# Optimization experiments

Measured on AMD Instinct MI355X. Metric: run time of the kernel, lower is better.

The kernel has to match this reference:

```python
import jax, jax.numpy as jnp
import numpy as np

B, S, T = 64, 256, 32
VS, VT = 4000, 32000
E = H = 512
L = 2
PAD_IDX = 1
BOS_IDX = 2


def setup_inputs() -> dict:
    key = jax.random.key(0)
    ks = jax.random.split(key, 16)
    u = lambda k, sh: jax.random.uniform(k, sh, jnp.float32, -0.08, 0.08)
    inp = {
        'X': jax.random.randint(ks[0], (B, S), 0, VS),
        'y': jax.random.randint(ks[1], (B, T), 0, VT),
        'emb_src': u(ks[2], (VS, E)).at[PAD_IDX].set(0.0),
        'emb_tgt': u(ks[3], (VT, E)).at[PAD_IDX].set(0.0),
        'enc_Wih': u(ks[4], (L, 4 * H, E)),
        'enc_Whh': u(ks[5], (L, 4 * H, H)),
        'enc_bih': u(ks[6], (L, 4 * H)),
        'enc_bhh': u(ks[7], (L, 4 * H)),
        'dec_Wih': u(ks[8], (L, 4 * H, E)),
        'dec_Whh': u(ks[9], (L, 4 * H, H)),
        'dec_bih': u(ks[10], (L, 4 * H)),
        'dec_bhh': u(ks[11], (L, 4 * H)),
        'fcW': u(ks[12], (VT, H)),
        'fcb': u(ks[13], (VT,)),
    }
    return inp


def _cell(x, h, c, Wih, Whh, bih, bhh):
    # PyTorch LSTM cell, gate order i,f,g,o. x:[B,E], h,c:[B,H]
    gates = x @ Wih.T + h @ Whh.T + bih + bhh  # [B,4H]
    i, f, g, o = jnp.split(gates, 4, axis=-1)
    c = jax.nn.sigmoid(f) * c + jax.nn.sigmoid(i) * jnp.tanh(g)
    h = jax.nn.sigmoid(o) * jnp.tanh(c)
    return h, c


def _stack_step(x, hs, cs, Wih, Whh, bih, bhh):
    # run num_layers stacked cells for one timestep; hs,cs: [L,B,H]
    new_h, new_c = [], []
    inp = x
    for l in range(Wih.shape[0]):
        h, c = _cell(inp, hs[l], cs[l], Wih[l], Whh[l], bih[l], bhh[l])
        new_h.append(h)
        new_c.append(c)
        inp = h
    return jnp.stack(new_h), jnp.stack(new_c), inp


def _forward(X, y, emb_src, emb_tgt, enc_Wih, enc_Whh, enc_bih, enc_bhh,
             dec_Wih, dec_Whh, dec_bih, dec_bhh, fcW, fcb):
    b = X.shape[0]
    # ----- encoder: LSTM over full (un-padded) source sequence -----
    xs = emb_src[X].transpose(1, 0, 2)  # [S,B,E] time-major
    h0 = jnp.zeros((L, b, H), xs.dtype)
    c0 = jnp.zeros((L, b, H), xs.dtype)

    def enc_step(carry, x):
        hs, cs = carry
        hs, cs, _ = _stack_step(x, hs, cs, enc_Wih, enc_Whh, enc_bih, enc_bhh)
        return (hs, cs), None

    (hs, cs), _ = jax.lax.scan(enc_step, (h0, c0), xs)

    bos = jnp.full((b, 1), BOS_IDX, y.dtype)
    dec_in = jnp.concatenate([bos, y[:, :-1]], axis=1)  # [B,T]
    toks = dec_in.transpose(1, 0)  # [T,B]

    def dec_step(carry, tok):
        hs, cs = carry
        x = emb_tgt[tok]  # [B,E]
        hs, cs, top = _stack_step(x, hs, cs, dec_Wih, dec_Whh, dec_bih, dec_bhh)
        return (hs, cs), top

    (_, _), tops = jax.lax.scan(dec_step, (hs, cs), toks)  # tops: [T,B,H]
    # model returns only the last time step's log-softmax prediction
    logits = tops[-1] @ fcW.T + fcb  # [B,VT]
    return jax.nn.log_softmax(logits, axis=-1)


def reference(X, y, emb_src, emb_tgt, enc_Wih, enc_Whh, enc_bih, enc_bhh,
              dec_Wih, dec_Whh, dec_bih, dec_bhh, fcW, fcb):
    return _forward(X, y, emb_src, emb_tgt, enc_Wih, enc_Whh, enc_bih, enc_bhh,
                    dec_Wih, dec_Whh, dec_bih, dec_bhh, fcW, fcb)
```

## Files before the change

### kernel.cpp

```cpp
#include <hip/hip_runtime.h>

#define NB 256
#define NT 256

typedef __attribute__((ext_vector_type(8))) short short8;
typedef __attribute__((ext_vector_type(4))) float f32x4;

constexpr int Bz = 64, Sz = 256, Tz = 32, Ez = 512, Hz = 512, G4 = 2048, VT = 32000;

__device__ __forceinline__ unsigned short f2b(float f) {
    unsigned u; __builtin_memcpy(&u, &f, 4);
    u = (u + 0x7fffu + ((u >> 16) & 1u)) >> 16;
    return (unsigned short)u;
}
__device__ __forceinline__ float sgm(float x) { return 1.0f / (1.0f + __expf(-x)); }
__device__ __forceinline__ float tnh(float x) { return 1.0f - 2.0f / (1.0f + __expf(2.0f * x)); }

__global__ __launch_bounds__(NT) void init_kernel(
    unsigned* __restrict__ hbuf_u32, float* __restrict__ row_sums,
    unsigned* __restrict__ bars)
{
    const int idx = blockIdx.x * NT + threadIdx.x;
#pragma unroll
    for (int i = 0; i < 4; ++i) hbuf_u32[idx * 4 + i] = 0u;
    if (blockIdx.x == 0) {
        bars[threadIdx.x] = 0u;
        if (threadIdx.x < 64) row_sums[threadIdx.x] = 0.0f;
    }
}

__global__ __launch_bounds__(NT, 2) void scan_kernel(
    const int* __restrict__ X, const int* __restrict__ Y,
    const float* __restrict__ emb_src, const float* __restrict__ emb_tgt,
    const float* __restrict__ eWih, const float* __restrict__ eWhh,
    const float* __restrict__ ebih, const float* __restrict__ ebhh,
    const float* __restrict__ dWih, const float* __restrict__ dWhh,
    const float* __restrict__ dbih, const float* __restrict__ dbhh,
    unsigned short* __restrict__ hbuf,
    unsigned* __restrict__ bars)
{
    __shared__ __align__(16) unsigned char smem[38144];
    unsigned short* xh_lds = (unsigned short*)smem;
    float* gates_lds = (float*)(smem + 33024);
    float* c_lds     = (float*)(smem + 33024 + 4096);

    const int tid  = threadIdx.x;
    const int bid  = blockIdx.x;
    const int lay  = bid >> 7;
    const int bt   = (bid >> 5) & 3;
    const int ht   = bid & 31;
    const int wave = tid >> 6;
    const int lane = tid & 63;
    const int nl   = lane & 15;
    const int quad = lane >> 4;
    const int srow = tid >> 4;
    const int ssub = tid & 15;
    const int bglob = bt * 16 + srow;

    unsigned* bar_arrive = bars + bt * 64;
    unsigned* bar_flag   = bars + bt * 64 + 32;
    unsigned gen = 0;

    auto barrier = [&]() {
        ++gen;
        __syncthreads();
        if (tid == 0) {
            unsigned old = __hip_atomic_fetch_add(bar_arrive, 1u,
                               __ATOMIC_RELAXED, __HIP_MEMORY_SCOPE_AGENT);
            if (old == gen * 64u - 1u) {
                __hip_atomic_store(bar_flag, gen,
                                   __ATOMIC_RELAXED, __HIP_MEMORY_SCOPE_AGENT);
            } else {
                while (__hip_atomic_load(bar_flag,
                           __ATOMIC_RELAXED, __HIP_MEMORY_SCOPE_AGENT) < gen)
                    __builtin_amdgcn_s_sleep(1);
            }
        }
        __syncthreads();
    };

    c_lds[tid] = 0.0f;
    __syncthreads();

    short8 wfrag[32];
    float bias_r = 0.0f;
    const int r = wave * 512 + ht * 16 + nl;

    auto load_w = [&](const float* Wih, const float* Whh,
                      const float* bih, const float* bhh) {
        const float* wi = Wih + (size_t)(lay * G4 + r) * 512;
        const float* wh = Whh + (size_t)(lay * G4 + r) * 512;
#pragma unroll
        for (int kc = 0; kc < 32; ++kc) {
            const int k0 = kc * 32 + quad * 8;
            const float* s = (k0 < 512) ? (wi + k0) : (wh + (k0 - 512));
            short8 v;
#pragma unroll
            for (int j = 0; j < 8; ++j) v[j] = (short)f2b(s[j]);
            wfrag[kc] = v;
        }
        bias_r = bih[lay * G4 + r] + bhh[lay * G4 + r];
    };

    auto step = [&](const float* xrow_f, const unsigned short* xrow_b,
                    const unsigned short* hrow, unsigned short* hout) {
        {
            unsigned short* d = xh_lds + srow * 1032;
            if (xrow_f) {
                short8* dx = (short8*)(d + ssub * 32);
                const float4* xs = (const float4*)xrow_f;
#pragma unroll
                for (int i = 0; i < 4; ++i) {
                    float4 lo = xs[ssub * 8 + 2 * i];
                    float4 hi = xs[ssub * 8 + 2 * i + 1];
                    short8 v;
                    v[0] = (short)f2b(lo.x); v[1] = (short)f2b(lo.y);
                    v[2] = (short)f2b(lo.z); v[3] = (short)f2b(lo.w);
                    v[4] = (short)f2b(hi.x); v[5] = (short)f2b(hi.y);
                    v[6] = (short)f2b(hi.z); v[7] = (short)f2b(hi.w);
                    dx[i] = v;
                }
            } else {
                const unsigned long long* xs = (const unsigned long long*)xrow_b;
                unsigned long long* dx = (unsigned long long*)(d + ssub * 32);
#pragma unroll
                for (int i = 0; i < 8; ++i)
                    dx[i] = __hip_atomic_load(xs + ssub * 8 + i,
                                __ATOMIC_RELAXED, __HIP_MEMORY_SCOPE_AGENT);
            }
            const unsigned long long* hs = (const unsigned long long*)hrow;
            unsigned long long* dh = (unsigned long long*)(d + 512 + ssub * 32);
#pragma unroll
            for (int i = 0; i < 8; ++i)
                dh[i] = __hip_atomic_load(hs + ssub * 8 + i,
                            __ATOMIC_RELAXED, __HIP_MEMORY_SCOPE_AGENT);
        }
        __syncthreads();
        f32x4 acc = {0.f, 0.f, 0.f, 0.f};
        const unsigned short* ar = xh_lds + nl * 1032 + quad * 8;
#pragma unroll
        for (int kc = 0; kc < 32; ++kc) {
            short8 a = *(const short8*)(ar + kc * 32);
            acc = __builtin_amdgcn_mfma_f32_16x16x32_bf16(a, wfrag[kc], acc, 0, 0, 0);
        }
#pragma unroll
        for (int i = 0; i < 4; ++i) {
            float v = acc[i] + bias_r;
            v = (wave == 2) ? tnh(v) : sgm(v);
            gates_lds[wave * 256 + (quad * 4 + i) * 16 + nl] = v;
        }
        __syncthreads();
        if (tid < 128) {
            const int m = tid >> 3, np = tid & 7;
            float hp[2];
#pragma unroll
            for (int j = 0; j < 2; ++j) {
                const int n = 2 * np + j;
                const float iv = gates_lds[      m * 16 + n];
                const float fv = gates_lds[256 + m * 16 + n];
                const float gv = gates_lds[512 + m * 16 + n];
                const float ov = gates_lds[768 + m * 16 + n];
                float c = c_lds[m * 16 + n];
                c = fv * c + iv * gv;
                c_lds[m * 16 + n] = c;
                hp[j] = ov * tnh(c);
            }
            const unsigned pack = (unsigned)f2b(hp[0]) | ((unsigned)f2b(hp[1]) << 16);
            unsigned* dst = (unsigned*)&hout[(bt * 16 + m) * 512 + ht * 16 + 2 * np];
            __hip_atomic_store(dst, pack, __ATOMIC_RELAXED, __HIP_MEMORY_SCOPE_AGENT);
        }
    };

    auto hb = [&](int l, int p) { return hbuf + (size_t)(l * 2 + p) * Bz * Hz; };

    load_w(eWih, eWhh, ebih, ebhh);
    for (int t = 0; t <= Sz; ++t) {
        if (lay == 0) {
            if (t < Sz) {
                const int tok = X[bglob * Sz + t];
                step(emb_src + (size_t)tok * Ez, nullptr,
                     hb(0, (t + 1) & 1) + bglob * Hz, hb(0, t & 1));
            }
        } else {
            if (t >= 1) {
                const int s = t - 1;
                step(nullptr, hb(0, s & 1) + bglob * Hz,
                     hb(1, (s + 1) & 1) + bglob * Hz, hb(1, s & 1));
            }
        }
        barrier();
    }

    load_w(dWih, dWhh, dbih, dbhh);
    for (int t = 0; t <= Tz; ++t) {
        if (lay == 0) {
            if (t < Tz) {
                const int tok = (t == 0) ? 2 : Y[bglob * Tz + t - 1];
                step(emb_tgt + (size_t)tok * Ez, nullptr,
                     hb(0, (t + 1) & 1) + bglob * Hz, hb(0, t & 1));
            }
        } else {
            if (t >= 1) {
                const int s = t - 1;
                step(nullptr, hb(0, s & 1) + bglob * Hz,
                     hb(1, (s + 1) & 1) + bglob * Hz, hb(1, s & 1));
            }
        }
        barrier();
    }
}

__global__ __launch_bounds__(NT, 1) void fc_kernel(
    const float* __restrict__ fcW, const float* __restrict__ fcb,
    const unsigned short* __restrict__ hbuf,
    float* __restrict__ logits, float* __restrict__ row_sums)
{
    __shared__ __align__(16) unsigned char smem[66816];
    unsigned short* h_lds = (unsigned short*)smem;
    float* row_part = (float*)(smem + 64 * 520 * 2);

    const int tid  = threadIdx.x;
    const int bid  = blockIdx.x;
    const int wave = tid >> 6;
    const int lane = tid & 63;
    const int nl   = lane & 15;
    const int quad = lane >> 4;

    {
        const unsigned short* htop = hbuf + (size_t)3 * Bz * Hz;
        const int rr2 = tid >> 2, pp = tid & 3;
        const short8* s = (const short8*)(htop + rr2 * 512 + pp * 128);
        short8* d = (short8*)(h_lds + rr2 * 520 + pp * 128);
#pragma unroll
        for (int i = 0; i < 16; ++i) d[i] = s[i];
    }
    if (tid < 64) row_part[tid] = 0.f;
    __syncthreads();

    const int c0 = bid * 128;
    f32x4 acc[8];
#pragma unroll
    for (int ct = 0; ct < 8; ++ct) acc[ct] = (f32x4){0.f, 0.f, 0.f, 0.f};
    const unsigned short* ar = h_lds + (wave * 16 + nl) * 520 + quad * 8;
    const float* bb = fcW + ((size_t)c0 + nl) * 512 + quad * 8;
    for (int kc = 0; kc < 16; ++kc) {
        short8 a = *(const short8*)(ar + kc * 32);
#pragma unroll
        for (int ct = 0; ct < 8; ++ct) {
            const float* bp = bb + (size_t)ct * 16 * 512 + kc * 32;
            float4 lo = *(const float4*)(bp);
            float4 hi = *(const float4*)(bp + 4);
            short8 b;
            b[0] = (short)f2b(lo.x); b[1] = (short)f2b(lo.y);
            b[2] = (short)f2b(lo.z); b[3] = (short)f2b(lo.w);
            b[4] = (short)f2b(hi.x); b[5] = (short)f2b(hi.y);
            b[6] = (short)f2b(hi.z); b[7] = (short)f2b(hi.w);
            acc[ct] = __builtin_amdgcn_mfma_f32_16x16x32_bf16(a, b, acc[ct], 0, 0, 0);
        }
    }
    float ls[4] = {0.f, 0.f, 0.f, 0.f};
#pragma unroll
    for (int ct = 0; ct < 8; ++ct) {
        const int col = c0 + ct * 16 + nl;
        const float bias = fcb[col];
#pragma unroll
        for (int i = 0; i < 4; ++i) {
            const float lg = acc[ct][i] + bias;
            logits[(size_t)(wave * 16 + quad * 4 + i) * VT + col] = lg;
            ls[i] += __expf(lg);
        }
    }
#pragma unroll
    for (int i = 0; i < 4; ++i)
        atomicAdd(&row_part[wave * 16 + quad * 4 + i], ls[i]);
    __syncthreads();
    if (tid < 64) atomicAdd(&row_sums[tid], row_part[tid]);
}

__global__ __launch_bounds__(NT) void norm_kernel(
    const float* __restrict__ logits, const float* __restrict__ row_sums,
    float* __restrict__ out)
{
    const int idx = blockIdx.x * NT + threadIdx.x;
    const int row = idx / VT;
    out[idx] = logits[idx] - __logf(row_sums[row]);
}

extern "C" void kernel_launch(void* const* d_in, const int* in_sizes, int n_in,
                              void* d_out, int out_size, void* d_ws, size_t ws_size,
                              hipStream_t stream) {
    const int* X = (const int*)d_in[0];
    const int* Y = (const int*)d_in[1];
    const float* emb_src = (const float*)d_in[2];
    const float* emb_tgt = (const float*)d_in[3];
    const float* eWih = (const float*)d_in[4];
    const float* eWhh = (const float*)d_in[5];
    const float* ebih = (const float*)d_in[6];
    const float* ebhh = (const float*)d_in[7];
    const float* dWih = (const float*)d_in[8];
    const float* dWhh = (const float*)d_in[9];
    const float* dbih = (const float*)d_in[10];
    const float* dbhh = (const float*)d_in[11];
    const float* fcW = (const float*)d_in[12];
    const float* fcb = (const float*)d_in[13];
    float* out = (float*)d_out;

    unsigned short* hbuf = (unsigned short*)d_ws;
    float* row_sums = (float*)((char*)d_ws + 262144);
    unsigned* bars  = (unsigned*)((char*)d_ws + 266240);
    float* logits   = (float*)((char*)d_ws + 524288);

    init_kernel<<<dim3(64), dim3(NT), 0, stream>>>((unsigned*)hbuf, row_sums, bars);

    void* args[] = {&X, &Y, &emb_src, &emb_tgt, &eWih, &eWhh, &ebih, &ebhh,
                    &dWih, &dWhh, &dbih, &dbhh, &hbuf, &bars};
    hipLaunchCooperativeKernel(reinterpret_cast<void*>(scan_kernel),
                               dim3(NB), dim3(NT), args, 0, stream);

    fc_kernel<<<dim3(VT / 128), dim3(NT), 0, stream>>>(fcW, fcb, hbuf, logits, row_sums);

    norm_kernel<<<dim3((Bz * VT) / NT), dim3(NT), 0, stream>>>(logits, row_sums, out);
}
```

Before: 1.670 ms.

## Replace atomic-counter barrier with per-block flags and prefetch next embedding row

The grid barrier no longer has every block atomically increment one counter and spin on a single flag. Each block now writes its generation to its own flag slot, and one wave polls all 64 slots with a ballot, which removes the serialized atomic round trip. Layer-0 blocks load and convert the next timestep's embedding row into registers before the barrier, so that gather latency leaves the critical path. The FC kernel also writes logits straight into the output and normalizes in place, dropping a workspace buffer and its extra read. The costs are more polling traffic, since 64 loads per spin replace one, and a few more registers held live for the prefetch.

```diff
diff --git a/kernel.cpp b/kernel.cpp
--- a/kernel.cpp
+++ b/kernel.cpp
@@ -57,24 +57,20 @@
     const int ssub = tid & 15;
     const int bglob = bt * 16 + srow;
 
-    unsigned* bar_arrive = bars + bt * 64;
-    unsigned* bar_flag   = bars + bt * 64 + 32;
+    unsigned* flags = bars + bt * 64;
+    const int g = (lay << 5) | ht;
     unsigned gen = 0;
 
     auto barrier = [&]() {
         ++gen;
+        asm volatile("s_waitcnt vmcnt(0)" ::: "memory");
         __syncthreads();
-        if (tid == 0) {
-            unsigned old = __hip_atomic_fetch_add(bar_arrive, 1u,
+        if (tid == 0)
+            __hip_atomic_store(flags + g, gen,
                                __ATOMIC_RELAXED, __HIP_MEMORY_SCOPE_AGENT);
-            if (old == gen * 64u - 1u) {
-                __hip_atomic_store(bar_flag, gen,
-                                   __ATOMIC_RELAXED, __HIP_MEMORY_SCOPE_AGENT);
-            } else {
-                while (__hip_atomic_load(bar_flag,
-                           __ATOMIC_RELAXED, __HIP_MEMORY_SCOPE_AGENT) < gen)
-                    __builtin_amdgcn_s_sleep(1);
-            }
+        if (tid < 64) {
+            while (__ballot(__hip_atomic_load(flags + tid, __ATOMIC_RELAXED,
+                                __HIP_MEMORY_SCOPE_AGENT) >= gen) != ~0ull) {}
         }
         __syncthreads();
     };
@@ -102,24 +98,30 @@
         bias_r = bih[lay * G4 + r] + bhh[lay * G4 + r];
     };
 
-    auto step = [&](const float* xrow_f, const unsigned short* xrow_b,
+    short8 xr[4];
+    auto prefetch_x = [&](const float* xrow) {
+        const float4* xs = (const float4*)xrow;
+#pragma unroll
+        for (int i = 0; i < 4; ++i) {
+            float4 lo = xs[ssub * 8 + 2 * i];
+            float4 hi = xs[ssub * 8 + 2 * i + 1];
+            short8 v;
+            v[0] = (short)f2b(lo.x); v[1] = (short)f2b(lo.y);
+            v[2] = (short)f2b(lo.z); v[3] = (short)f2b(lo.w);
+            v[4] = (short)f2b(hi.x); v[5] = (short)f2b(hi.y);
+            v[6] = (short)f2b(hi.z); v[7] = (short)f2b(hi.w);
+            xr[i] = v;
+        }
+    };
+
+    auto step = [&](bool use_xr, const unsigned short* xrow_b,
                     const unsigned short* hrow, unsigned short* hout) {
         {
             unsigned short* d = xh_lds + srow * 1032;
-            if (xrow_f) {
+            if (use_xr) {
                 short8* dx = (short8*)(d + ssub * 32);
-                const float4* xs = (const float4*)xrow_f;
-#pragma unroll
-                for (int i = 0; i < 4; ++i) {
-                    float4 lo = xs[ssub * 8 + 2 * i];
-                    float4 hi = xs[ssub * 8 + 2 * i + 1];
-                    short8 v;
-                    v[0] = (short)f2b(lo.x); v[1] = (short)f2b(lo.y);
-                    v[2] = (short)f2b(lo.z); v[3] = (short)f2b(lo.w);
-                    v[4] = (short)f2b(hi.x); v[5] = (short)f2b(hi.y);
-                    v[6] = (short)f2b(hi.z); v[7] = (short)f2b(hi.w);
-                    dx[i] = v;
-                }
+#pragma unroll
+                for (int i = 0; i < 4; ++i) dx[i] = xr[i];
             } else {
                 const unsigned long long* xs = (const unsigned long long*)xrow_b;
                 unsigned long long* dx = (unsigned long long*)(d + ssub * 32);
@@ -174,17 +176,19 @@
     auto hb = [&](int l, int p) { return hbuf + (size_t)(l * 2 + p) * Bz * Hz; };
 
     load_w(eWih, eWhh, ebih, ebhh);
+    if (lay == 0) prefetch_x(emb_src + (size_t)X[bglob * Sz] * Ez);
     for (int t = 0; t <= Sz; ++t) {
         if (lay == 0) {
-            if (t < Sz) {
-                const int tok = X[bglob * Sz + t];
-                step(emb_src + (size_t)tok * Ez, nullptr,
-                     hb(0, (t + 1) & 1) + bglob * Hz, hb(0, t & 1));
-            }
+            if (t < Sz)
+                step(true, nullptr, hb(0, (t + 1) & 1) + bglob * Hz, hb(0, t & 1));
+            if (t + 1 < Sz)
+                prefetch_x(emb_src + (size_t)X[bglob * Sz + t + 1] * Ez);
+            else if (t + 1 == Sz)
+                prefetch_x(emb_tgt + (size_t)2 * Ez);
         } else {
             if (t >= 1) {
                 const int s = t - 1;
-                step(nullptr, hb(0, s & 1) + bglob * Hz,
+                step(false, hb(0, s & 1) + bglob * Hz,
                      hb(1, (s + 1) & 1) + bglob * Hz, hb(1, s & 1));
             }
         }
@@ -194,15 +198,14 @@
     load_w(dWih, dWhh, dbih, dbhh);
     for (int t = 0; t <= Tz; ++t) {
         if (lay == 0) {
-            if (t < Tz) {
-                const int tok = (t == 0) ? 2 : Y[bglob * Tz + t - 1];
-                step(emb_tgt + (size_t)tok * Ez, nullptr,
-                     hb(0, (t + 1) & 1) + bglob * Hz, hb(0, t & 1));
-            }
+            if (t < Tz)
+                step(true, nullptr, hb(0, (t + 1) & 1) + bglob * Hz, hb(0, t & 1));
+            if (t + 1 < Tz)
+                prefetch_x(emb_tgt + (size_t)Y[bglob * Tz + t] * Ez);
         } else {
             if (t >= 1) {
                 const int s = t - 1;
-                step(nullptr, hb(0, s & 1) + bglob * Hz,
+                step(false, hb(0, s & 1) + bglob * Hz,
                      hb(1, (s + 1) & 1) + bglob * Hz, hb(1, s & 1));
             }
         }
@@ -278,12 +281,11 @@
 }
 
 __global__ __launch_bounds__(NT) void norm_kernel(
-    const float* __restrict__ logits, const float* __restrict__ row_sums,
-    float* __restrict__ out)
+    const float* __restrict__ row_sums, float* __restrict__ out)
 {
     const int idx = blockIdx.x * NT + threadIdx.x;
     const int row = idx / VT;
-    out[idx] = logits[idx] - __logf(row_sums[row]);
+    out[idx] = out[idx] - __logf(row_sums[row]);
 }
 
 extern "C" void kernel_launch(void* const* d_in, const int* in_sizes, int n_in,
@@ -308,7 +310,6 @@
     unsigned short* hbuf = (unsigned short*)d_ws;
     float* row_sums = (float*)((char*)d_ws + 262144);
     unsigned* bars  = (unsigned*)((char*)d_ws + 266240);
-    float* logits   = (float*)((char*)d_ws + 524288);
 
     init_kernel<<<dim3(64), dim3(NT), 0, stream>>>((unsigned*)hbuf, row_sums, bars);
 
@@ -317,7 +318,7 @@
     hipLaunchCooperativeKernel(reinterpret_cast<void*>(scan_kernel),
                                dim3(NB), dim3(NT), args, 0, stream);
 
-    fc_kernel<<<dim3(VT / 128), dim3(NT), 0, stream>>>(fcW, fcb, hbuf, logits, row_sums);
-
-    norm_kernel<<<dim3((Bz * VT) / NT), dim3(NT), 0, stream>>>(logits, row_sums, out);
-}
+    fc_kernel<<<dim3(VT / 128), dim3(NT), 0, stream>>>(fcW, fcb, hbuf, out, row_sums);
+
+    norm_kernel<<<dim3((Bz * VT) / NT), dim3(NT), 0, stream>>>(row_sums, out);
+}
```

Measured after the change: 2.071 ms. 1.24x slower.
